# Performance work log

Measured on AMD Instinct MI355X. Metric: run time of the kernel, lower is better.

Reference implementation:

```python
import jax, jax.numpy as jnp
import numpy as np

EDGE_TYPES = 5
D = 256      # input_dim == output_dim
HID = 128    # hard-coded hidden size of agg MLPs


def setup_inputs() -> dict:
    key = jax.random.key(0)
    ks = jax.random.split(key, 8)
    B, E, N = 4, 8000, 2000
    edge_distribution = jax.random.uniform(ks[0], (B, E, EDGE_TYPES), dtype=jnp.float32)
    H = jax.random.normal(ks[1], (B, E, N), dtype=jnp.float32)
    ori = jax.random.normal(ks[2], (B, N, D), dtype=jnp.float32)
    # Stacked per-edge-type MLP params: Linear(D->128), ReLU, Linear(128->D)
    W1 = jax.random.normal(ks[3], (EDGE_TYPES, D, HID), dtype=jnp.float32) * (1.0 / np.sqrt(D))
    b1 = jax.random.normal(ks[4], (EDGE_TYPES, HID), dtype=jnp.float32) * 0.01
    W2 = jax.random.normal(ks[5], (EDGE_TYPES, HID, D), dtype=jnp.float32) * (1.0 / np.sqrt(HID))
    b2 = jax.random.normal(ks[6], (EDGE_TYPES, D), dtype=jnp.float32) * 0.01
    return {"edge_distribution": edge_distribution, "H": H, "ori": ori,
            "W1": W1, "b1": b1, "W2": W2, "b2": b2}


def reference(edge_distribution, H, ori, W1, b1, W2, b2):
    # edges = H @ ori : [B, E, D]
    edges = jnp.matmul(H, ori)
    # Per-edge-type 2-layer MLP, vectorized over the type axis t
    h = jax.nn.relu(jnp.einsum('bed,tdh->tbeh', edges, W1) + b1[:, None, None, :])  # [T,B,E,HID]
    mlp_out = jnp.einsum('tbeh,thd->tbed', h, W2) + b2[:, None, None, :]            # [T,B,E,D]
    # Gated accumulate: sum_t edge_distribution[...,t] * mlp_out[t]
    edge_feature = jnp.einsum('bet,tbed->bed', edge_distribution, mlp_out)          # [B,E,D]
    # node_feature = concat(H^T @ edge_feature, ori)
    node_feature = jnp.concatenate(
        [jnp.matmul(jnp.swapaxes(H, 1, 2), edge_feature), ori], axis=-1)            # [B,N,2D]
    return node_feature
```

## Files before the change

kernel.cpp:

```cpp
#include <hip/hip_runtime.h>
#include <hip/hip_bf16.h>

typedef unsigned short u16;
typedef short bf16x8 __attribute__((ext_vector_type(8)));
typedef float f32x4 __attribute__((ext_vector_type(4)));
typedef unsigned short u16x8 __attribute__((ext_vector_type(8)));

#define GLL16(gp, lp) __builtin_amdgcn_global_load_lds( \
    (__attribute__((address_space(1))) const unsigned int*)(gp), \
    (__attribute__((address_space(3))) unsigned int*)(lp), 16, 0, 0)

static __device__ __forceinline__ u16 f2bf(float f){
  return __builtin_bit_cast(u16, __float2bfloat16(f));
}

__global__ void transpose_f32(const float* __restrict__ src, u16* __restrict__ dst,
                              int R, int C, int Rpad, long sB, long dB){
  __shared__ u16 tile[32][33];
  const int b = blockIdx.z;
  src += (long)b*sB; dst += (long)b*dB;
  const int r0 = blockIdx.x*32, c0 = blockIdx.y*32;
  const int j = threadIdx.x & 31, i0 = threadIdx.x >> 5;
  #pragma unroll
  for (int ii=0; ii<32; ii+=8){
    int r = r0+i0+ii, c = c0+j;
    u16 v = 0;
    if (r < R && c < C) v = f2bf(src[(long)r*C + c]);
    tile[i0+ii][j] = v;
  }
  __syncthreads();
  #pragma unroll
  for (int ii=0; ii<32; ii+=8){
    int c = c0+i0+ii, r = r0+j;
    if (c < C && r < Rpad) dst[(long)c*Rpad + r] = tile[j][i0+ii];
  }
}

__global__ __launch_bounds__(512,2) void g1mlp_kernel(
    const float* __restrict__ Hm, const u16* __restrict__ oriT,
    const u16* __restrict__ W1T, const u16* __restrict__ W2T,
    const float* __restrict__ b1, const float* __restrict__ b2,
    const float* __restrict__ edist, u16* __restrict__ HT, u16* __restrict__ EFt){
  __shared__ __align__(16) char smem[141312];
  u16*   Bs  = (u16*)(smem);
  float* eds = (float*)(smem + 32768);
  float* b1s = (float*)(smem + 35328);
  float* b2s = (float*)(smem + 37888);
  u16*   As  = (u16*)(smem + 43008);
  u16*   At  = (u16*)(smem + 59392);
  u16*   Es  = (u16*)(smem + 43008);
  u16*   Hs  = (u16*)(smem + 108544);

  const int b = blockIdx.y, bm = blockIdx.x*128;
  const int tid = threadIdx.x;
  const int w = tid>>6, quad = (tid&63)>>4, l16 = tid&15;
  const int wm = (w&1)*64, wn = (w>>1)*64;
  const float* Ab = Hm + (size_t)b*8000*2000 + (size_t)bm*2000;
  const u16*  Bb = oriT + (size_t)b*256*2048;
  u16* HTb = HT + (size_t)b*2048*8000;
  const bool edge_blk = (bm == 7936);

  for (int i=tid;i<640;i+=512){
    int e = bm + i/5;
    eds[i] = (e < 8000) ? edist[((size_t)b*8000 + bm)*5 + i] : 0.f;
  }
  for (int i=tid;i<640;i+=512)  b1s[i] = b1[i];
  for (int i=tid;i<1280;i+=512) b2s[i] = b2[i];

  float4 pa[2];
  auto loadA = [&](int kt, bool guard){
    const int k0 = kt*32;
    #pragma unroll
    for (int i=0;i<2;i++){
      int idx = i*512+tid, row = idx>>3, c4 = (idx&7)*4;
      if (!guard){
        pa[i] = *(const float4*)(Ab + (size_t)row*2000 + k0+c4);
      } else {
        bool ok = (bm+row < 8000) && (k0+c4 < 2000);
        pa[i] = ok ? *(const float4*)(Ab + (size_t)row*2000 + k0+c4) : make_float4(0.f,0.f,0.f,0.f);
      }
    }
  };
  auto storeA = [&](int kt){
    const int buf = kt&1;
    #pragma unroll
    for (int i=0;i<2;i++){
      int idx = i*512+tid, row = idx>>3, c4 = (idx&7)*4;
      ushort4 o; o.x=f2bf(pa[i].x); o.y=f2bf(pa[i].y); o.z=f2bf(pa[i].z); o.w=f2bf(pa[i].w);
      *(ushort4*)(&As[buf*4096 + idx*4]) = o;
      At[buf*4352 + (c4+0)*136 + (row ^ ((((c4+0)>>3)&3)<<3))] = o.x;
      At[buf*4352 + (c4+1)*136 + (row ^ ((((c4+1)>>3)&3)<<3))] = o.y;
      At[buf*4352 + (c4+2)*136 + (row ^ ((((c4+2)>>3)&3)<<3))] = o.z;
      At[buf*4352 + (c4+3)*136 + (row ^ ((((c4+3)>>3)&3)<<3))] = o.w;
    }
  };
  auto stageB = [&](int kt){
    const int buf = kt&1, k0 = kt*32;
    #pragma unroll
    for (int i=0;i<2;i++){
      int idx = i*512+tid;
      int row = idx>>2, c8 = (idx&3)*8;
      GLL16(Bb + (size_t)row*2048 + k0+c8, &Bs[buf*8192 + (i*512 + w*64)*8]);
    }
  };

  f32x4 acc[4][4];
  #pragma unroll
  for (int i=0;i<4;i++)
    #pragma unroll
    for (int j=0;j<4;j++) acc[i][j] = (f32x4){0.f,0.f,0.f,0.f};

  loadA(0, edge_blk); stageB(0);
  for (int kt=0; kt<64; kt++){
    storeA(kt);
    __syncthreads();
    if (kt+1 < 64){ loadA(kt+1, edge_blk || (kt+1 >= 62)); stageB(kt+1); }
    const int buf = kt&1, k0 = kt*32;
    {
      int kk = tid>>4, c = tid&15, m0 = c*8;
      if (bm + m0 < 8000){
        u16x8 v = *(const u16x8*)(&At[buf*4352 + kk*136 + (m0 ^ (((kk>>3)&3)<<3))]);
        *(u16x8*)(HTb + (size_t)(k0+kk)*8000 + bm + m0) = v;
      }
    }
    bf16x8 af[4], bf[4];
    #pragma unroll
    for (int mi=0;mi<4;mi++) af[mi] = *(const bf16x8*)(&As[buf*4096 + (wm+mi*16+l16)*32 + quad*8]);
    #pragma unroll
    for (int ni=0;ni<4;ni++) bf[ni] = *(const bf16x8*)(&Bs[buf*8192 + (wn+ni*16+l16)*32 + quad*8]);
    #pragma unroll
    for (int mi=0;mi<4;mi++)
      #pragma unroll
      for (int ni=0;ni<4;ni++)
        acc[mi][ni] = __builtin_amdgcn_mfma_f32_16x16x32_bf16(af[mi], bf[ni], acc[mi][ni], 0,0,0);
  }

  __syncthreads();
  {
    int row = tid>>2, c8 = (tid&3)*8;
    GLL16(W1T + (size_t)row*256 + c8, &Bs[0*8192 + (w*64)*8]);
  }
  #pragma unroll
  for (int mi=0;mi<4;mi++){
    #pragma unroll
    for (int r=0;r<4;r++){
      int m = wm + mi*16 + quad*4 + r;
      #pragma unroll
      for (int ni=0;ni<4;ni++){
        int d = wn + ni*16 + l16;
        Es[(d>>5)*4096 + m*32 + (d&31)] = f2bf(acc[mi][ni][r]);
      }
    }
  }
  __syncthreads();

  const int wm1 = (w&1)*64, wh1 = ((w>>1)&3)*32;
  const int wd2 = (w&3)*64, wm2 = (w>>2)*64;

  auto stageW1 = [&](int t, int kt){
    const int buf = kt&1;
    int row = tid>>2, c8 = (tid&3)*8;
    GLL16(W1T + ((size_t)t*128 + row)*256 + kt*32 + c8, &Bs[buf*8192 + (w*64)*8]);
  };
  auto stageW2 = [&](int t, int kk){
    const int buf = kk&1;
    #pragma unroll
    for (int i=0;i<2;i++){
      int idx = i*512+tid, row = idx>>2, c8 = (idx&3)*8;
      GLL16(W2T + ((size_t)t*256 + row)*128 + kk*32 + c8, &Bs[buf*8192 + (i*512 + w*64)*8]);
    }
  };

  f32x4 acc2[4][4];
  #pragma unroll
  for (int i=0;i<4;i++)
    #pragma unroll
    for (int j=0;j<4;j++) acc2[i][j] = (f32x4){0.f,0.f,0.f,0.f};

  for (int t=0;t<5;t++){
    f32x4 acc1[4][2];
    #pragma unroll
    for (int i=0;i<4;i++){ acc1[i][0] = (f32x4){0.f,0.f,0.f,0.f}; acc1[i][1] = (f32x4){0.f,0.f,0.f,0.f}; }
    for (int kt=0;kt<8;kt++){
      if (kt<7) stageW1(t,kt+1); else stageW2(t,0);
      const int buf = kt&1;
      bf16x8 af[4], bfr[2];
      #pragma unroll
      for (int mi=0;mi<4;mi++) af[mi] = *(const bf16x8*)(&Es[kt*4096 + (wm1+mi*16+l16)*32 + quad*8]);
      #pragma unroll
      for (int ni=0;ni<2;ni++) bfr[ni] = *(const bf16x8*)(&Bs[buf*8192 + (wh1+ni*16+l16)*32 + quad*8]);
      #pragma unroll
      for (int mi=0;mi<4;mi++)
        #pragma unroll
        for (int ni=0;ni<2;ni++)
          acc1[mi][ni] = __builtin_amdgcn_mfma_f32_16x16x32_bf16(af[mi], bfr[ni], acc1[mi][ni], 0,0,0);
      __syncthreads();
    }
    #pragma unroll
    for (int mi=0;mi<4;mi++){
      #pragma unroll
      for (int r=0;r<4;r++){
        int lrow = wm1 + mi*16 + quad*4 + r;
        float s = eds[lrow*5 + t];
        #pragma unroll
        for (int ni=0;ni<2;ni++){
          int ch = wh1 + ni*16 + l16;
          float v = fmaxf(acc1[mi][ni][r] + b1s[t*128 + ch], 0.f) * s;
          Hs[(ch>>5)*4096 + lrow*32 + (ch&31)] = f2bf(v);
        }
      }
    }
    __syncthreads();
    for (int kk=0;kk<4;kk++){
      if (kk<3) stageW2(t,kk+1); else if (t<4) stageW1(t+1,0);
      const int buf = kk&1;
      bf16x8 af2[4], bf2[4];
      #pragma unroll
      for (int mi=0;mi<4;mi++) af2[mi] = *(const bf16x8*)(&Bs[buf*8192 + (wd2+mi*16+l16)*32 + quad*8]);
      #pragma unroll
      for (int ni=0;ni<4;ni++) bf2[ni] = *(const bf16x8*)(&Hs[kk*4096 + (wm2+ni*16+l16)*32 + quad*8]);
      #pragma unroll
      for (int mi=0;mi<4;mi++)
        #pragma unroll
        for (int ni=0;ni<4;ni++)
          acc2[mi][ni] = __builtin_amdgcn_mfma_f32_16x16x32_bf16(af2[mi], bf2[ni], acc2[mi][ni], 0,0,0);
      __syncthreads();
    }
  }
  #pragma unroll
  for (int mi=0;mi<4;mi++){
    #pragma unroll
    for (int r=0;r<4;r++){
      int d = wd2 + mi*16 + quad*4 + r;
      #pragma unroll
      for (int ni=0;ni<4;ni++){
        int mc = wm2 + ni*16 + l16;
        int e = bm + mc;
        if (e < 8000){
          float bias = eds[mc*5+0]*b2s[d] + eds[mc*5+1]*b2s[256+d] + eds[mc*5+2]*b2s[512+d]
                     + eds[mc*5+3]*b2s[768+d] + eds[mc*5+4]*b2s[1024+d];
          EFt[((size_t)b*256 + d)*8000 + e] = f2bf(acc2[mi][ni][r] + bias);
        }
      }
    }
  }
}

__global__ __launch_bounds__(512,2) void g3_kernel(
    const u16* __restrict__ HT, const u16* __restrict__ EFt, float* __restrict__ part){
  __shared__ u16 As[2][128*32];
  __shared__ u16 Bs[2][256*32];
  const int wg = ((int)blockIdx.x & 7)*32 + ((int)blockIdx.x >> 3);
  const int bm = (wg & 15)*128, ks = (wg>>4)&3, b = wg>>6;
  const int tid = threadIdx.x;
  const int w = tid>>6, quad = (tid&63)>>4, l16 = tid&15;
  const int wm = (w&1)*64, wn = (w>>1)*64;
  const u16* Ab = HT + (size_t)b*2048*8000 + (size_t)bm*8000;
  const u16* Bb = EFt + (size_t)b*256*8000;
  const int it0 = (250*ks)/4, it1 = (250*(ks+1))/4;

  auto stage = [&](int kt){
    const int buf = kt&1, k0 = kt*32;
    {
      int row = tid>>2, c8 = (tid&3)*8;
      GLL16(Ab + (size_t)row*8000 + k0+c8, &As[buf][(w*64)*8]);
    }
    #pragma unroll
    for (int i=0;i<2;i++){
      int idx = i*512+tid, row = idx>>2, c8 = (idx&3)*8;
      GLL16(Bb + (size_t)row*8000 + k0+c8, &Bs[buf][(i*512 + w*64)*8]);
    }
  };

  f32x4 acc[4][4];
  #pragma unroll
  for (int i=0;i<4;i++)
    #pragma unroll
    for (int j=0;j<4;j++) acc[i][j] = (f32x4){0.f,0.f,0.f,0.f};

  stage(it0);
  for (int kt=it0; kt<it1; kt++){
    __syncthreads();
    if (kt+1 < it1) stage(kt+1);
    const int buf = kt&1;
    bf16x8 af[4], bf[4];
    #pragma unroll
    for (int mi=0;mi<4;mi++) af[mi] = *(const bf16x8*)(&As[buf][(wm+mi*16+l16)*32 + quad*8]);
    #pragma unroll
    for (int ni=0;ni<4;ni++) bf[ni] = *(const bf16x8*)(&Bs[buf][(wn+ni*16+l16)*32 + quad*8]);
    #pragma unroll
    for (int mi=0;mi<4;mi++)
      #pragma unroll
      for (int ni=0;ni<4;ni++)
        acc[mi][ni] = __builtin_amdgcn_mfma_f32_16x16x32_bf16(af[mi], bf[ni], acc[mi][ni], 0,0,0);
  }
  float* dst0 = part + ((size_t)(b*4 + ks)*2048)*256;
  #pragma unroll
  for (int mi=0;mi<4;mi++){
    #pragma unroll
    for (int r=0;r<4;r++){
      int gm = bm + wm + mi*16 + quad*4 + r;
      float* dst = dst0 + (size_t)gm*256;
      #pragma unroll
      for (int ni=0;ni<4;ni++) dst[wn + ni*16 + l16] = acc[mi][ni][r];
    }
  }
}

__global__ void assemble_kernel(const float* __restrict__ part, const float* __restrict__ ori,
                                float* __restrict__ out){
  const int b = blockIdx.y;
  int u = blockIdx.x*256 + threadIdx.x;
  int n = u>>6, c4 = (u&63)*4;
  f32x4 s = (f32x4){0.f,0.f,0.f,0.f};
  #pragma unroll
  for (int ks=0; ks<4; ks++)
    s += *(const f32x4*)(part + ((size_t)(b*4+ks)*2048 + n)*256 + c4);
  float* dst = out + ((size_t)(b*2000+n))*512;
  *(f32x4*)(dst + c4) = s;
  *(f32x4*)(dst + 256 + c4) = *(const f32x4*)(ori + ((size_t)(b*2000+n))*256 + c4);
}

extern "C" void kernel_launch(void* const* d_in, const int* in_sizes, int n_in,
                              void* d_out, int out_size, void* d_ws, size_t ws_size,
                              hipStream_t stream) {
  const float* ed  = (const float*)d_in[0];
  const float* Hm  = (const float*)d_in[1];
  const float* ori = (const float*)d_in[2];
  const float* W1  = (const float*)d_in[3];
  const float* b1  = (const float*)d_in[4];
  const float* W2  = (const float*)d_in[5];
  const float* b2  = (const float*)d_in[6];
  float* out = (float*)d_out;
  char* ws = (char*)d_ws;

  u16* HT    = (u16*)(ws);
  u16* oriT  = (u16*)(ws + 131072000);
  u16* W1T   = (u16*)(ws + 135266304);
  u16* W2T   = (u16*)(ws + 135593984);
  u16* EFt   = (u16*)(ws + 152305664);
  float* part = (float*)(ws + 168689664);

  hipLaunchKernelGGL(transpose_f32, dim3(64,8,4), dim3(256), 0, stream,
                     ori, oriT, 2000, 256, 2048, 512000L, 524288L);
  hipLaunchKernelGGL(transpose_f32, dim3(8,4,5), dim3(256), 0, stream,
                     W1, W1T, 256, 128, 256, 32768L, 32768L);
  hipLaunchKernelGGL(transpose_f32, dim3(4,8,5), dim3(256), 0, stream,
                     W2, W2T, 128, 256, 128, 32768L, 32768L);

  hipLaunchKernelGGL(g1mlp_kernel, dim3(63,4), dim3(512), 0, stream,
                     Hm, oriT, W1T, W2T, b1, b2, ed, HT, EFt);
  hipLaunchKernelGGL(g3_kernel, dim3(256), dim3(512), 0, stream, HT, EFt, part);
  hipLaunchKernelGGL(assemble_kernel, dim3(500,4), dim3(256), 0, stream, part, ori, out);

  (void)in_sizes; (void)n_in; (void)ws_size;
}
```

Before: 529.2 us.

## Deepen A prefetch, load MLP weights directly from global, shrink LDS

The first GEMM loop is unrolled by two and uses two register buffers for the H tiles, so global loads are issued two k-steps ahead. The MLP phases stop staging W1/W2 through LDS with global_load_lds and instead read the weight fragments straight from global memory (expected to hit L2), which removes the per-k-step barriers in those loops. LDS is shrunk from about 141 KB to 109 KB, which could let more blocks fit per CU. The cost is more registers for the extra prefetch buffer and higher latency on the global weight reads.

```diff
diff --git a/kernel.cpp b/kernel.cpp
--- a/kernel.cpp
+++ b/kernel.cpp
@@ -41,15 +41,15 @@
     const u16* __restrict__ W1T, const u16* __restrict__ W2T,
     const float* __restrict__ b1, const float* __restrict__ b2,
     const float* __restrict__ edist, u16* __restrict__ HT, u16* __restrict__ EFt){
-  __shared__ __align__(16) char smem[141312];
-  u16*   Bs  = (u16*)(smem);
-  float* eds = (float*)(smem + 32768);
-  float* b1s = (float*)(smem + 35328);
-  float* b2s = (float*)(smem + 37888);
-  u16*   As  = (u16*)(smem + 43008);
-  u16*   At  = (u16*)(smem + 59392);
-  u16*   Es  = (u16*)(smem + 43008);
-  u16*   Hs  = (u16*)(smem + 108544);
+  __shared__ __align__(16) char smem[109568];
+  float* eds = (float*)(smem);
+  float* b1s = (float*)(smem + 2560);
+  float* b2s = (float*)(smem + 5120);
+  u16*   As  = (u16*)(smem + 10240);
+  u16*   At  = (u16*)(smem + 26624);
+  u16*   Bs  = (u16*)(smem + 44032);
+  u16*   Es  = (u16*)(smem + 10240);
+  u16*   Hs  = (u16*)(smem + 76800);
 
   const int b = blockIdx.y, bm = blockIdx.x*128;
   const int tid = threadIdx.x;
@@ -67,26 +67,26 @@
   for (int i=tid;i<640;i+=512)  b1s[i] = b1[i];
   for (int i=tid;i<1280;i+=512) b2s[i] = b2[i];
 
-  float4 pa[2];
-  auto loadA = [&](int kt, bool guard){
+  float4 paA[2], paB[2];
+  auto loadA = [&](int kt, float4 (&p)[2], bool guard){
     const int k0 = kt*32;
     #pragma unroll
     for (int i=0;i<2;i++){
       int idx = i*512+tid, row = idx>>3, c4 = (idx&7)*4;
       if (!guard){
-        pa[i] = *(const float4*)(Ab + (size_t)row*2000 + k0+c4);
+        p[i] = *(const float4*)(Ab + (size_t)row*2000 + k0+c4);
       } else {
         bool ok = (bm+row < 8000) && (k0+c4 < 2000);
-        pa[i] = ok ? *(const float4*)(Ab + (size_t)row*2000 + k0+c4) : make_float4(0.f,0.f,0.f,0.f);
+        p[i] = ok ? *(const float4*)(Ab + (size_t)row*2000 + k0+c4) : make_float4(0.f,0.f,0.f,0.f);
       }
     }
   };
-  auto storeA = [&](int kt){
+  auto storeA = [&](int kt, float4 (&p)[2]){
     const int buf = kt&1;
     #pragma unroll
     for (int i=0;i<2;i++){
       int idx = i*512+tid, row = idx>>3, c4 = (idx&7)*4;
-      ushort4 o; o.x=f2bf(pa[i].x); o.y=f2bf(pa[i].y); o.z=f2bf(pa[i].z); o.w=f2bf(pa[i].w);
+      ushort4 o; o.x=f2bf(p[i].x); o.y=f2bf(p[i].y); o.z=f2bf(p[i].z); o.w=f2bf(p[i].w);
       *(ushort4*)(&As[buf*4096 + idx*4]) = o;
       At[buf*4352 + (c4+0)*136 + (row ^ ((((c4+0)>>3)&3)<<3))] = o.x;
       At[buf*4352 + (c4+1)*136 + (row ^ ((((c4+1)>>3)&3)<<3))] = o.y;
@@ -103,6 +103,14 @@
       GLL16(Bb + (size_t)row*2048 + k0+c8, &Bs[buf*8192 + (i*512 + w*64)*8]);
     }
   };
+  auto htwrite = [&](int kt){
+    const int buf = kt&1, k0 = kt*32;
+    int kk = tid>>4, c = tid&15, m0 = c*8;
+    if (bm + m0 < 8000){
+      u16x8 v = *(const u16x8*)(&At[buf*4352 + kk*136 + (m0 ^ (((kk>>3)&3)<<3))]);
+      *(u16x8*)(HTb + (size_t)(k0+kk)*8000 + bm + m0) = v;
+    }
+  };
 
   f32x4 acc[4][4];
   #pragma unroll
@@ -110,19 +118,7 @@
     #pragma unroll
     for (int j=0;j<4;j++) acc[i][j] = (f32x4){0.f,0.f,0.f,0.f};
 
-  loadA(0, edge_blk); stageB(0);
-  for (int kt=0; kt<64; kt++){
-    storeA(kt);
-    __syncthreads();
-    if (kt+1 < 64){ loadA(kt+1, edge_blk || (kt+1 >= 62)); stageB(kt+1); }
-    const int buf = kt&1, k0 = kt*32;
-    {
-      int kk = tid>>4, c = tid&15, m0 = c*8;
-      if (bm + m0 < 8000){
-        u16x8 v = *(const u16x8*)(&At[buf*4352 + kk*136 + (m0 ^ (((kk>>3)&3)<<3))]);
-        *(u16x8*)(HTb + (size_t)(k0+kk)*8000 + bm + m0) = v;
-      }
-    }
+  auto domfma = [&](int buf){
     bf16x8 af[4], bf[4];
     #pragma unroll
     for (int mi=0;mi<4;mi++) af[mi] = *(const bf16x8*)(&As[buf*4096 + (wm+mi*16+l16)*32 + quad*8]);
@@ -133,13 +129,25 @@
       #pragma unroll
       for (int ni=0;ni<4;ni++)
         acc[mi][ni] = __builtin_amdgcn_mfma_f32_16x16x32_bf16(af[mi], bf[ni], acc[mi][ni], 0,0,0);
+  };
+
+  loadA(0, paA, edge_blk); loadA(1, paB, edge_blk); stageB(0);
+  for (int kt=0; kt<64; kt+=2){
+    storeA(kt, paA);
+    __syncthreads();
+    if (kt+2 < 64) loadA(kt+2, paA, edge_blk || (kt+2 >= 62));
+    stageB(kt+1);
+    htwrite(kt);
+    domfma(0);
+    storeA(kt+1, paB);
+    __syncthreads();
+    if (kt+3 < 64) loadA(kt+3, paB, edge_blk || (kt+3 >= 62));
+    if (kt+2 < 64) stageB(kt+2);
+    htwrite(kt+1);
+    domfma(1);
   }
 
   __syncthreads();
-  {
-    int row = tid>>2, c8 = (tid&3)*8;
-    GLL16(W1T + (size_t)row*256 + c8, &Bs[0*8192 + (w*64)*8]);
-  }
   #pragma unroll
   for (int mi=0;mi<4;mi++){
     #pragma unroll
@@ -157,20 +165,6 @@
   const int wm1 = (w&1)*64, wh1 = ((w>>1)&3)*32;
   const int wd2 = (w&3)*64, wm2 = (w>>2)*64;
 
-  auto stageW1 = [&](int t, int kt){
-    const int buf = kt&1;
-    int row = tid>>2, c8 = (tid&3)*8;
-    GLL16(W1T + ((size_t)t*128 + row)*256 + kt*32 + c8, &Bs[buf*8192 + (w*64)*8]);
-  };
-  auto stageW2 = [&](int t, int kk){
-    const int buf = kk&1;
-    #pragma unroll
-    for (int i=0;i<2;i++){
-      int idx = i*512+tid, row = idx>>2, c8 = (idx&3)*8;
-      GLL16(W2T + ((size_t)t*256 + row)*128 + kk*32 + c8, &Bs[buf*8192 + (i*512 + w*64)*8]);
-    }
-  };
-
   f32x4 acc2[4][4];
   #pragma unroll
   for (int i=0;i<4;i++)
@@ -181,21 +175,21 @@
     f32x4 acc1[4][2];
     #pragma unroll
     for (int i=0;i<4;i++){ acc1[i][0] = (f32x4){0.f,0.f,0.f,0.f}; acc1[i][1] = (f32x4){0.f,0.f,0.f,0.f}; }
+    #pragma unroll
     for (int kt=0;kt<8;kt++){
-      if (kt<7) stageW1(t,kt+1); else stageW2(t,0);
-      const int buf = kt&1;
       bf16x8 af[4], bfr[2];
       #pragma unroll
+      for (int ni=0;ni<2;ni++)
+        bfr[ni] = *(const bf16x8*)(W1T + ((size_t)t*128 + wh1+ni*16+l16)*256 + kt*32 + quad*8);
+      #pragma unroll
       for (int mi=0;mi<4;mi++) af[mi] = *(const bf16x8*)(&Es[kt*4096 + (wm1+mi*16+l16)*32 + quad*8]);
-      #pragma unroll
-      for (int ni=0;ni<2;ni++) bfr[ni] = *(const bf16x8*)(&Bs[buf*8192 + (wh1+ni*16+l16)*32 + quad*8]);
       #pragma unroll
       for (int mi=0;mi<4;mi++)
         #pragma unroll
         for (int ni=0;ni<2;ni++)
           acc1[mi][ni] = __builtin_amdgcn_mfma_f32_16x16x32_bf16(af[mi], bfr[ni], acc1[mi][ni], 0,0,0);
-      __syncthreads();
-    }
+    }
+    __syncthreads();
     #pragma unroll
     for (int mi=0;mi<4;mi++){
       #pragma unroll
@@ -211,12 +205,12 @@
       }
     }
     __syncthreads();
+    #pragma unroll
     for (int kk=0;kk<4;kk++){
-      if (kk<3) stageW2(t,kk+1); else if (t<4) stageW1(t+1,0);
-      const int buf = kk&1;
       bf16x8 af2[4], bf2[4];
       #pragma unroll
-      for (int mi=0;mi<4;mi++) af2[mi] = *(const bf16x8*)(&Bs[buf*8192 + (wd2+mi*16+l16)*32 + quad*8]);
+      for (int mi=0;mi<4;mi++)
+        af2[mi] = *(const bf16x8*)(W2T + ((size_t)t*256 + wd2+mi*16+l16)*128 + kk*32 + quad*8);
       #pragma unroll
       for (int ni=0;ni<4;ni++) bf2[ni] = *(const bf16x8*)(&Hs[kk*4096 + (wm2+ni*16+l16)*32 + quad*8]);
       #pragma unroll
@@ -224,7 +218,6 @@
         #pragma unroll
         for (int ni=0;ni<4;ni++)
           acc2[mi][ni] = __builtin_amdgcn_mfma_f32_16x16x32_bf16(af2[mi], bf2[ni], acc2[mi][ni], 0,0,0);
-      __syncthreads();
     }
   }
   #pragma unroll
```

New measurement: 540.5 us. 1.02x slower.
